# Performance work log

Measured on AMD Instinct MI355X. Metric: run time of the kernel, lower is better.

Reference implementation:

```python
import jax, jax.numpy as jnp
import numpy as np

B, F, L, P, H = 32, 64, 8192, 96, 8
HD = F // H
EPS_ATTN = 1e-6
EPS_REVIN = 1e-5
EPS_LN = 1e-5


def setup_inputs() -> dict:
    key = jax.random.key(0)
    ks = jax.random.split(key, 8)
    f32 = jnp.float32
    return {
        'x': jax.random.normal(ks[0], (B, F, L), dtype=f32),
        'gamma': jnp.ones((1, 1, F), dtype=f32),
        'beta': jnp.zeros((1, 1, F), dtype=f32),
        'ln_w': jnp.ones((F,), dtype=f32),
        'ln_b': jnp.zeros((F,), dtype=f32),
        'Wq': 0.05 * jax.random.normal(ks[1], (F, F), dtype=f32),
        'bq': jnp.zeros((F,), dtype=f32),
        'Wk': 0.05 * jax.random.normal(ks[2], (F, F), dtype=f32),
        'bk': jnp.zeros((F,), dtype=f32),
        'Wv': 0.05 * jax.random.normal(ks[3], (F, F), dtype=f32),
        'bv': jnp.zeros((F,), dtype=f32),
        'Wo': 0.05 * jax.random.normal(ks[4], (F, F), dtype=f32),
        'bo': jnp.zeros((F,), dtype=f32),
        'Wlin': 0.01 * jax.random.normal(ks[5], (P, L), dtype=f32),
        'blin': jnp.zeros((P,), dtype=f32),
        'Wp': 0.1 * jax.random.normal(ks[6], (1, F), dtype=f32),
        'bp': jnp.zeros((1,), dtype=f32),
    }


def _phi(t):
    # feature map: elu(x) + 1 (non-negative)
    return jax.nn.elu(t) + 1.0


def _layernorm(h, w, b):
    mu = jnp.mean(h, axis=-1, keepdims=True)
    var = jnp.mean(jnp.square(h - mu), axis=-1, keepdims=True)
    return (h - mu) * jax.lax.rsqrt(var + EPS_LN) * w + b


def reference(x, gamma, beta, ln_w, ln_b, Wq, bq, Wk, bk, Wv, bv, Wo, bo,
              Wlin, blin, Wp, bp):
    # (B, F, L) -> (B, L, F)
    xt = jnp.transpose(x, (0, 2, 1))
    # RevIN norm (stats over time axis, detached; torch std is unbiased ddof=1)
    mean = jax.lax.stop_gradient(jnp.mean(xt, axis=1, keepdims=True))
    std = jax.lax.stop_gradient(jnp.std(xt, axis=1, keepdims=True, ddof=1) + EPS_REVIN)
    xn = (xt - mean) / std * gamma + beta
    residual = xn
    h = _layernorm(xn, ln_w, ln_b)
    # Q/K/V projections (torch Linear: h @ W.T + b)
    Q = h @ Wq.T + bq
    K = h @ Wk.T + bk
    V = h @ Wv.T + bv
    # (B, L, F) -> (B, H, L, HD)
    def heads(t):
        return jnp.transpose(t.reshape(B, L, H, HD), (0, 2, 1, 3))
    Q, K, V = heads(Q), heads(K), heads(V)
    Q, K = _phi(Q), _phi(K)
    # linear attention: phi(Q) (phi(K)^T V) / (phi(Q) sum_n phi(K))
    KV = jnp.einsum('bhnd,bhne->bhde', K, V)           # (B,H,HD,HD)
    out = jnp.einsum('bhnd,bhde->bhne', Q, KV)          # (B,H,L,HD)
    Z = jnp.sum(K, axis=2)                              # (B,H,HD)
    normalizer = jnp.einsum('bhnd,bhd->bhn', Q, Z)[..., None] + EPS_ATTN
    out = out / normalizer
    out = jnp.transpose(out, (0, 2, 1, 3)).reshape(B, L, F)
    out = out @ Wo.T + bo
    y = out + residual                                  # (B, L, F)
    # temporal linear: (B, F, L) @ Wlin.T -> (B, F, P) -> (B, P, F)
    y = jnp.transpose(jnp.transpose(y, (0, 2, 1)) @ Wlin.T + blin, (0, 2, 1))
    # RevIN denorm
    y = (y - beta) / gamma
    y = y * std + mean
    # projector to scalar per step
    return (y @ Wp.T + bp)[..., 0]                      # (B, P)
```

## Files before the change

kernel.cpp:

```cpp
#include <hip/hip_runtime.h>
#include <cstddef>

#define NB 32
#define NF 64
#define NL 8192
#define NP 96
#define NH 8
#define TSPLIT 32

#define WS_MEAN 0
#define WS_STD  2048
#define WS_RSTD 4096
#define WS_KV   6144
#define WS_Z    22528
#define WS_OUT2 24576
#define WS_MUN  221184
#define WS_RSN  483328
#define WS_WLB  745472
#define WS_XNB  1138688
#define WS_YT   9527296

typedef __bf16 bfx8 __attribute__((ext_vector_type(8)));
typedef float f32x4 __attribute__((ext_vector_type(4)));
#define MFMA16(a, b, c) __builtin_amdgcn_mfma_f32_16x16x32_bf16((a), (b), (c), 0, 0, 0)

__device__ __forceinline__ unsigned short f2bf(float f) {
  unsigned u = __float_as_uint(f);
  unsigned r = u + 0x7FFFu + ((u >> 16) & 1u);
  return (unsigned short)(r >> 16);
}
__device__ __forceinline__ unsigned packbf2(float lo, float hi) {
  return (unsigned)f2bf(lo) | ((unsigned)f2bf(hi) << 16);
}
__device__ __forceinline__ float bflo(unsigned d) { return __uint_as_float(d << 16); }
__device__ __forceinline__ float bfhi(unsigned d) { return __uint_as_float(d & 0xFFFF0000u); }
__device__ __forceinline__ float bf1(unsigned short s) { return __uint_as_float(((unsigned)s) << 16); }

__device__ __forceinline__ bfx8 ldfrag(const unsigned short* p) {
  uint4 u = *(const uint4*)p;
  return __builtin_bit_cast(bfx8, u);
}

__global__ __launch_bounds__(256) void k_stats(const float* __restrict__ x,
                                               float* __restrict__ wmean,
                                               float* __restrict__ wstd,
                                               float* __restrict__ wrstd) {
  int bf = blockIdx.x;
  int tid = threadIdx.x;
  const float4* row4 = (const float4*)(x + (size_t)bf * NL);
  float s1 = 0.f, s2 = 0.f;
#pragma unroll
  for (int i = 0; i < NL / 4 / 256; i++) {
    float4 v = row4[tid + i * 256];
    s1 += v.x + v.y + v.z + v.w;
    s2 += v.x * v.x + v.y * v.y + v.z * v.z + v.w * v.w;
  }
  __shared__ float r1[256], r2[256];
  r1[tid] = s1; r2[tid] = s2;
  __syncthreads();
  for (int off = 128; off > 0; off >>= 1) {
    if (tid < off) { r1[tid] += r1[tid + off]; r2[tid] += r2[tid + off]; }
    __syncthreads();
  }
  if (tid == 0) {
    float m = r1[0] * (1.f / NL);
    float var = (r2[0] - (float)NL * m * m) * (1.f / (NL - 1));
    float sd = sqrtf(fmaxf(var, 0.f)) + 1e-5f;
    wmean[bf] = m;
    wstd[bf] = sd;
    wrstd[bf] = 1.f / sd;
  }
}

__global__ __launch_bounds__(256) void k_wlb(const float* __restrict__ Wlin,
                                             unsigned short* __restrict__ wlb) {
  int i = blockIdx.x * 256 + threadIdx.x;
  int p = i >> 10;
  int l8 = (i & 1023) * 8;
  float4 va = *(const float4*)&Wlin[(size_t)p * NL + l8];
  float4 vb = *(const float4*)&Wlin[(size_t)p * NL + l8 + 4];
  uint4 o;
  o.x = packbf2(va.x, va.y); o.y = packbf2(va.z, va.w);
  o.z = packbf2(vb.x, vb.y); o.w = packbf2(vb.z, vb.w);
  *(uint4*)&wlb[(((size_t)(l8 >> 5)) * NP + p) * 32 + (l8 & 31)] = o;
}

__global__ __launch_bounds__(256, 4) void k_kv(
    const float* __restrict__ x,
    const float* __restrict__ gamma, const float* __restrict__ beta,
    const float* __restrict__ lnw, const float* __restrict__ lnb,
    const float* __restrict__ Wk, const float* __restrict__ bk,
    const float* __restrict__ Wv, const float* __restrict__ bv,
    const float* __restrict__ wmean, const float* __restrict__ wrstd,
    float* __restrict__ wKV, float* __restrict__ wZ,
    float* __restrict__ wmun, float* __restrict__ wrsn,
    unsigned short* __restrict__ xnb) {
  __shared__ __align__(16) char smem[40960];
  unsigned short* hA  = (unsigned short*)smem;
  unsigned short* WkB = (unsigned short*)(smem + 18432);
  unsigned short* WvB = (unsigned short*)(smem + 27648);
  unsigned short* pK  = (unsigned short*)smem;
  unsigned short* pV  = (unsigned short*)(smem + 17408);
  float* SkT   = (float*)(smem + 36864);
  float* Tpart = (float*)(smem + 37888);
  float* mun   = (float*)(smem + 39936);
  float* rsn   = (float*)(smem + 40448);

  const int tid = threadIdx.x;
  const int b = blockIdx.x >> 6;
  const int tI = blockIdx.x & 63;
  const int L0 = tI * 128;
  const int lane = tid & 63, wv = tid >> 6;
  const int mm = lane & 15, qd = lane >> 4;

  {
    int jj = tid >> 2, g = tid & 3;
    int f0 = g * 16;
    float tkp = 0.f, tvp = 0.f;
#pragma unroll
    for (int i = 0; i < 4; i++) {
      int f = f0 + i * 4;
      float4 wk4 = *(const float4*)&Wk[jj * NF + f];
      float4 wv4 = *(const float4*)&Wv[jj * NF + f];
      float4 lw  = *(const float4*)&lnw[f];
      float4 lb  = *(const float4*)&lnb[f];
      uint2 pk2, pv2;
      pk2.x = packbf2(wk4.x * lw.x, wk4.y * lw.y);
      pk2.y = packbf2(wk4.z * lw.z, wk4.w * lw.w);
      pv2.x = packbf2(wv4.x * lw.x, wv4.y * lw.y);
      pv2.y = packbf2(wv4.z * lw.z, wv4.w * lw.w);
      *(uint2*)&WkB[jj * 72 + f] = pk2;
      *(uint2*)&WvB[jj * 72 + f] = pv2;
      tkp += lb.x * wk4.x + lb.y * wk4.y + lb.z * wk4.z + lb.w * wk4.w;
      tvp += lb.x * wv4.x + lb.y * wv4.y + lb.z * wv4.z + lb.w * wv4.w;
    }
    Tpart[g * 64 + jj] = tkp;
    Tpart[256 + g * 64 + jj] = tvp;
  }

  if (tid < 128) {
    float xn[NF];
    float mu = 0.f;
#pragma unroll
    for (int f = 0; f < NF; f++) {
      float v = x[((size_t)(b * NF + f)) * NL + L0 + tid];
      v = (v - wmean[b * NF + f]) * wrstd[b * NF + f] * gamma[f] + beta[f];
      xn[f] = v; mu += v;
    }
    mu *= (1.f / NF);
    float var = 0.f;
#pragma unroll
    for (int f = 0; f < NF; f++) { float d = xn[f] - mu; var += d * d; }
    float rs = rsqrtf(var * (1.f / NF) + 1e-5f);
    mun[tid] = mu; rsn[tid] = rs;
    wmun[(size_t)b * NL + L0 + tid] = mu;
    wrsn[(size_t)b * NL + L0 + tid] = rs;
    unsigned* hrow = (unsigned*)&hA[tid * 72];
#pragma unroll
    for (int f2 = 0; f2 < 32; f2++)
      hrow[f2] = packbf2(xn[2 * f2], xn[2 * f2 + 1]);
  }
  __syncthreads();

  {
    int row = tid >> 1, half = tid & 1;
    const uint4* s4 = (const uint4*)&hA[row * 72 + half * 32];
    uint4* d4 = (uint4*)(xnb + (((size_t)(b * 64 + tI) * 128 + row) * 64 + half * 32));
    d4[0] = s4[0]; d4[1] = s4[1]; d4[2] = s4[2]; d4[3] = s4[3];
  }

  if (tid < 128) {
    int sel = tid >> 6, j = tid & 63;
    const unsigned* wr = (const unsigned*)((sel ? WvB : WkB) + j * 72);
    float s = 0.f;
#pragma unroll
    for (int i = 0; i < 32; i++) { unsigned d = wr[i]; s += bflo(d) + bfhi(d); }
    float t = Tpart[sel * 256 + j] + Tpart[sel * 256 + 64 + j] +
              Tpart[sel * 256 + 128 + j] + Tpart[sel * 256 + 192 + j];
    t += sel ? bv[j] : bk[j];
    SkT[sel * 128 + j] = s;
    SkT[sel * 128 + 64 + j] = t;
  }
  __syncthreads();

  const f32x4 fz = {0.f, 0.f, 0.f, 0.f};
  f32x4 kacc[2][4], vacc[2][4];
#pragma unroll
  for (int i = 0; i < 2; i++)
#pragma unroll
    for (int jt = 0; jt < 4; jt++) { kacc[i][jt] = fz; vacc[i][jt] = fz; }

#pragma unroll
  for (int kc = 0; kc < 2; kc++) {
    bfx8 a0 = ldfrag(&hA[(wv * 32 + mm) * 72 + kc * 32 + qd * 8]);
    bfx8 a1 = ldfrag(&hA[(wv * 32 + 16 + mm) * 72 + kc * 32 + qd * 8]);
#pragma unroll
    for (int jt = 0; jt < 4; jt++) {
      bfx8 bkf = ldfrag(&WkB[(jt * 16 + mm) * 72 + kc * 32 + qd * 8]);
      bfx8 bvf = ldfrag(&WvB[(jt * 16 + mm) * 72 + kc * 32 + qd * 8]);
      kacc[0][jt] = MFMA16(a0, bkf, kacc[0][jt]);
      kacc[1][jt] = MFMA16(a1, bkf, kacc[1][jt]);
      vacc[0][jt] = MFMA16(a0, bvf, vacc[0][jt]);
      vacc[1][jt] = MFMA16(a1, bvf, vacc[1][jt]);
    }
  }

#pragma unroll
  for (int lt2 = 0; lt2 < 2; lt2++) {
    float4 mu4 = *(const float4*)&mun[wv * 32 + lt2 * 16 + qd * 4];
    float4 rs4 = *(const float4*)&rsn[wv * 32 + lt2 * 16 + qd * 4];
    float muv[4] = {mu4.x, mu4.y, mu4.z, mu4.w};
    float rsv[4] = {rs4.x, rs4.y, rs4.z, rs4.w};
#pragma unroll
    for (int jt = 0; jt < 4; jt++) {
      int j = jt * 16 + mm;
      float Sk = SkT[j], Tk = SkT[64 + j], Sv = SkT[128 + j], Tv = SkT[192 + j];
#pragma unroll
      for (int r = 0; r < 4; r++) {
        float kk = rsv[r] * (kacc[lt2][jt][r] - muv[r] * Sk) + Tk;
        kacc[lt2][jt][r] = (kk > 0.f) ? (kk + 1.f) : __expf(kk);
        vacc[lt2][jt][r] = rsv[r] * (vacc[lt2][jt][r] - muv[r] * Sv) + Tv;
      }
    }
  }
  __syncthreads();

#pragma unroll
  for (int lt2 = 0; lt2 < 2; lt2++) {
    int l0 = wv * 32 + lt2 * 16 + qd * 4;
#pragma unroll
    for (int jt = 0; jt < 4; jt++) {
      int j = jt * 16 + mm;
      uint2 dk, dv;
      dk.x = packbf2(kacc[lt2][jt][0], kacc[lt2][jt][1]);
      dk.y = packbf2(kacc[lt2][jt][2], kacc[lt2][jt][3]);
      dv.x = packbf2(vacc[lt2][jt][0], vacc[lt2][jt][1]);
      dv.y = packbf2(vacc[lt2][jt][2], vacc[lt2][jt][3]);
      *(uint2*)&pK[j * 136 + l0] = dk;
      *(uint2*)&pV[j * 136 + l0] = dv;
    }
  }
  __syncthreads();

  {
    f32x4 racc = fz;
#pragma unroll
    for (int kb = 0; kb < 4; kb++) {
      bfx8 ak = ldfrag(&pK[(wv * 16 + mm) * 136 + kb * 32 + qd * 8]);
      bfx8 bv8 = ldfrag(&pV[(wv * 16 + mm) * 136 + kb * 32 + qd * 8]);
      racc = MFMA16(ak, bv8, racc);
    }
    int eh = mm >> 3, e = mm & 7;
#pragma unroll
    for (int r = 0; r < 4; r++) {
      int row = qd * 4 + r;
      if ((row >> 3) == eh)
        atomicAdd(&wKV[(b * NH + wv * 2 + eh) * 64 + (row & 7) * 8 + e], racc[r]);
    }
  }
  if (tid < 64) {
    const unsigned* kr = (const unsigned*)&pK[tid * 136];
    float zs = 0.f;
#pragma unroll
    for (int i = 0; i < 64; i++) { unsigned d = kr[i]; zs += bflo(d) + bfhi(d); }
    atomicAdd(&wZ[b * 64 + tid], zs);
  }
}

__global__ __launch_bounds__(256, 3) void k_qy(
    const unsigned short* __restrict__ xnb,
    const float* __restrict__ lnw, const float* __restrict__ lnb,
    const float* __restrict__ Wq, const float* __restrict__ bq,
    const float* __restrict__ Wo, const float* __restrict__ bo,
    const float* __restrict__ wmun, const float* __restrict__ wrsn,
    const float* __restrict__ wKV, const float* __restrict__ wZ,
    unsigned short* __restrict__ ytb) {
  __shared__ __align__(16) char smem[41728];
  unsigned short* hA  = (unsigned short*)smem;
  unsigned short* qaA = (unsigned short*)smem;
  unsigned short* WqB = (unsigned short*)(smem + 18432);
  unsigned short* WoB = (unsigned short*)(smem + 27648);
  float* kvz   = (float*)(smem + 36864);
  float* mun   = (float*)(smem + 39168);
  float* rsn   = (float*)(smem + 39680);
  float* SqTq  = (float*)(smem + 40192);
  float* Tpart = (float*)(smem + 40704);

  const int tid = threadIdx.x;
  const int b = blockIdx.x >> 6;
  const int tI = blockIdx.x & 63;
  const int L0 = tI * 128;
  const int lane = tid & 63, wv = tid >> 6;
  const int mm = lane & 15, qd = lane >> 4;
  const unsigned short* xtile = xnb + (size_t)(b * 64 + tI) * 128 * 64;

  {
    int jj = tid >> 2, g = tid & 3;
    int f0 = g * 16;
    float tqp = 0.f;
#pragma unroll
    for (int i = 0; i < 4; i++) {
      int f = f0 + i * 4;
      float4 wq4 = *(const float4*)&Wq[jj * NF + f];
      float4 wo4 = *(const float4*)&Wo[jj * NF + f];
      float4 lw  = *(const float4*)&lnw[f];
      float4 lb  = *(const float4*)&lnb[f];
      uint2 pq2, po2;
      pq2.x = packbf2(wq4.x * lw.x, wq4.y * lw.y);
      pq2.y = packbf2(wq4.z * lw.z, wq4.w * lw.w);
      po2.x = packbf2(wo4.x, wo4.y);
      po2.y = packbf2(wo4.z, wo4.w);
      *(uint2*)&WqB[jj * 72 + f] = pq2;
      *(uint2*)&WoB[jj * 72 + f] = po2;
      tqp += lb.x * wq4.x + lb.y * wq4.y + lb.z * wq4.z + lb.w * wq4.w;
    }
    Tpart[g * 64 + jj] = tqp;
  }
  for (int i = tid; i < 576; i += 256)
    kvz[i] = (i < 512) ? wKV[b * 512 + i] : wZ[b * 64 + i - 512];
  {
    int row = tid >> 1, half = tid & 1;
    const uint4* s4 = (const uint4*)(xtile + (size_t)row * 64 + half * 32);
    uint4 u0 = s4[0], u1 = s4[1], u2 = s4[2], u3 = s4[3];
    uint4* d4 = (uint4*)&hA[row * 72 + half * 32];
    d4[0] = u0; d4[1] = u1; d4[2] = u2; d4[3] = u3;
  }
  if (tid < 128) {
    mun[tid] = wmun[(size_t)b * NL + L0 + tid];
    rsn[tid] = wrsn[(size_t)b * NL + L0 + tid];
  }
  __syncthreads();

  if (tid < 64) {
    const unsigned* wr = (const unsigned*)(WqB + tid * 72);
    float s = 0.f;
#pragma unroll
    for (int i = 0; i < 32; i++) { unsigned d = wr[i]; s += bflo(d) + bfhi(d); }
    float t = Tpart[tid] + Tpart[64 + tid] + Tpart[128 + tid] + Tpart[192 + tid] + bq[tid];
    SqTq[tid] = s; SqTq[64 + tid] = t;
  }
  __syncthreads();

  const f32x4 fz = {0.f, 0.f, 0.f, 0.f};

  {
    f32x4 qacc[2][4];
#pragma unroll
    for (int i = 0; i < 2; i++)
#pragma unroll
      for (int jt = 0; jt < 4; jt++) qacc[i][jt] = fz;
#pragma unroll
    for (int kc = 0; kc < 2; kc++) {
      bfx8 a0 = ldfrag(&hA[(wv * 32 + mm) * 72 + kc * 32 + qd * 8]);
      bfx8 a1 = ldfrag(&hA[(wv * 32 + 16 + mm) * 72 + kc * 32 + qd * 8]);
#pragma unroll
      for (int jt = 0; jt < 4; jt++) {
        bfx8 bqf = ldfrag(&WqB[(jt * 16 + mm) * 72 + kc * 32 + qd * 8]);
        qacc[0][jt] = MFMA16(a0, bqf, qacc[0][jt]);
        qacc[1][jt] = MFMA16(a1, bqf, qacc[1][jt]);
      }
    }
#pragma unroll
    for (int lt2 = 0; lt2 < 2; lt2++) {
      float4 mu4 = *(const float4*)&mun[wv * 32 + lt2 * 16 + qd * 4];
      float4 rs4 = *(const float4*)&rsn[wv * 32 + lt2 * 16 + qd * 4];
      float muv[4] = {mu4.x, mu4.y, mu4.z, mu4.w};
      float rsv[4] = {rs4.x, rs4.y, rs4.z, rs4.w};
      int l0 = wv * 32 + lt2 * 16 + qd * 4;
#pragma unroll
      for (int jt = 0; jt < 4; jt++) {
        int j = jt * 16 + mm;
        float Sj = SqTq[j], Tj = SqTq[64 + j];
#pragma unroll
        for (int r = 0; r < 4; r++) {
          float q = rsv[r] * (qacc[lt2][jt][r] - muv[r] * Sj) + Tj;
          q = (q > 0.f) ? (q + 1.f) : __expf(q);
          qaA[(l0 + r) * 72 + j] = f2bf(q);
        }
      }
    }
  }
  __syncthreads();

  {
    int lt = tid & 31, hd = tid >> 5;
    int lbase = lt * 4;
    float qv[4][8];
#pragma unroll
    for (int i = 0; i < 4; i++) {
      uint4 u = *(const uint4*)&qaA[(lbase + i) * 72 + hd * 8];
      qv[i][0] = bflo(u.x); qv[i][1] = bfhi(u.x);
      qv[i][2] = bflo(u.y); qv[i][3] = bfhi(u.y);
      qv[i][4] = bflo(u.z); qv[i][5] = bfhi(u.z);
      qv[i][6] = bflo(u.w); qv[i][7] = bfhi(u.w);
    }
    float att[4][8], nrm[4];
#pragma unroll
    for (int i = 0; i < 4; i++) {
      nrm[i] = 1e-6f;
#pragma unroll
      for (int e = 0; e < 8; e++) att[i][e] = 0.f;
    }
#pragma unroll
    for (int d = 0; d < 8; d++) {
      float zd = kvz[512 + hd * 8 + d];
      float4 kva = *(const float4*)&kvz[hd * 64 + d * 8];
      float4 kvb = *(const float4*)&kvz[hd * 64 + d * 8 + 4];
#pragma unroll
      for (int i = 0; i < 4; i++) {
        float qq = qv[i][d];
        nrm[i] = fmaf(qq, zd, nrm[i]);
        att[i][0] = fmaf(qq, kva.x, att[i][0]);
        att[i][1] = fmaf(qq, kva.y, att[i][1]);
        att[i][2] = fmaf(qq, kva.z, att[i][2]);
        att[i][3] = fmaf(qq, kva.w, att[i][3]);
        att[i][4] = fmaf(qq, kvb.x, att[i][4]);
        att[i][5] = fmaf(qq, kvb.y, att[i][5]);
        att[i][6] = fmaf(qq, kvb.z, att[i][6]);
        att[i][7] = fmaf(qq, kvb.w, att[i][7]);
      }
    }
#pragma unroll
    for (int i = 0; i < 4; i++) {
      float inv = 1.f / nrm[i];
      uint4 o;
      o.x = packbf2(att[i][0] * inv, att[i][1] * inv);
      o.y = packbf2(att[i][2] * inv, att[i][3] * inv);
      o.z = packbf2(att[i][4] * inv, att[i][5] * inv);
      o.w = packbf2(att[i][6] * inv, att[i][7] * inv);
      *(uint4*)&qaA[(lbase + i) * 72 + hd * 8] = o;
    }
  }
  __syncthreads();

  {
    f32x4 yacc[2][4];
#pragma unroll
    for (int i = 0; i < 2; i++)
#pragma unroll
      for (int ft = 0; ft < 4; ft++) yacc[i][ft] = fz;
#pragma unroll
    for (int ec = 0; ec < 2; ec++) {
      bfx8 a0 = ldfrag(&qaA[(wv * 32 + mm) * 72 + ec * 32 + qd * 8]);
      bfx8 a1 = ldfrag(&qaA[(wv * 32 + 16 + mm) * 72 + ec * 32 + qd * 8]);
#pragma unroll
      for (int ft = 0; ft < 4; ft++) {
        bfx8 bof = ldfrag(&WoB[(ft * 16 + mm) * 72 + ec * 32 + qd * 8]);
        yacc[0][ft] = MFMA16(a0, bof, yacc[0][ft]);
        yacc[1][ft] = MFMA16(a1, bof, yacc[1][ft]);
      }
    }
#pragma unroll
    for (int lt2 = 0; lt2 < 2; lt2++) {
      int l0 = wv * 32 + lt2 * 16 + qd * 4;
#pragma unroll
      for (int ft = 0; ft < 4; ft++) {
        int ff = ft * 16 + mm;
        float bof = bo[ff];
        float v0 = yacc[lt2][ft][0] + bf1(xtile[(size_t)(l0 + 0) * 64 + ff]) + bof;
        float v1 = yacc[lt2][ft][1] + bf1(xtile[(size_t)(l0 + 1) * 64 + ff]) + bof;
        float v2 = yacc[lt2][ft][2] + bf1(xtile[(size_t)(l0 + 2) * 64 + ff]) + bof;
        float v3 = yacc[lt2][ft][3] + bf1(xtile[(size_t)(l0 + 3) * 64 + ff]) + bof;
        uint2 o2;
        o2.x = packbf2(v0, v1);
        o2.y = packbf2(v2, v3);
        size_t idx = (((size_t)b * (NL / 32) + (L0 >> 5) + wv) * 64 + ff) * 32 + lt2 * 16 + qd * 4;
        *(uint2*)&ytb[idx] = o2;
      }
    }
  }
}

__global__ __launch_bounds__(256) void k_temporal(
    const unsigned short* __restrict__ ytb, const unsigned short* __restrict__ wlb,
    float* __restrict__ out2) {
  const int tid = threadIdx.x, lane = tid & 63, wvx = tid >> 6;
  const int mm = lane & 15, qd = lane >> 4;
  const int b = blockIdx.x / TSPLIT;
  const int kc = blockIdx.x % TSPLIT;
  const f32x4 fz = {0.f, 0.f, 0.f, 0.f};
  f32x4 acc[6];
#pragma unroll
  for (int pt = 0; pt < 6; pt++) acc[pt] = fz;

#pragma unroll 2
  for (int ks = 0; ks < 8; ks++) {
    int lg = kc * 8 + ks;
    bfx8 bfr = ldfrag(&ytb[(((size_t)b * (NL / 32) + lg) * 64 + wvx * 16 + mm) * 32 + qd * 8]);
#pragma unroll
    for (int pt = 0; pt < 6; pt++) {
      bfx8 afr = ldfrag(&wlb[((size_t)lg * NP + pt * 16 + mm) * 32 + qd * 8]);
      acc[pt] = MFMA16(afr, bfr, acc[pt]);
    }
  }
  const int ff = wvx * 16 + mm;
#pragma unroll
  for (int pt = 0; pt < 6; pt++) {
#pragma unroll
    for (int r = 0; r < 4; r++) {
      int p = pt * 16 + qd * 4 + r;
      atomicAdd(&out2[((size_t)(b * NP + p)) * NF + ff], acc[pt][r]);
    }
  }
}

__global__ __launch_bounds__(64) void k_final(
    const float* __restrict__ out2, const float* __restrict__ blin,
    const float* __restrict__ gamma, const float* __restrict__ beta,
    const float* __restrict__ wmean, const float* __restrict__ wstd,
    const float* __restrict__ Wp, const float* __restrict__ bp,
    float* __restrict__ out) {
  int b = blockIdx.x / NP;
  int p = blockIdx.x % NP;
  int f = threadIdx.x;
  float v = out2[((size_t)(b * NP + p)) * NF + f] + blin[p];
  v = (v - beta[f]) / gamma[f];
  v = v * wstd[b * NF + f] + wmean[b * NF + f];
  float s = v * Wp[f];
#pragma unroll
  for (int off = 32; off > 0; off >>= 1)
    s += __shfl_down(s, off, 64);
  if (f == 0) out[blockIdx.x] = s + bp[0];
}

extern "C" void kernel_launch(void* const* d_in, const int* in_sizes, int n_in,
                              void* d_out, int out_size, void* d_ws, size_t ws_size,
                              hipStream_t stream) {
  const float* x     = (const float*)d_in[0];
  const float* gamma = (const float*)d_in[1];
  const float* beta  = (const float*)d_in[2];
  const float* lnw   = (const float*)d_in[3];
  const float* lnb   = (const float*)d_in[4];
  const float* Wq    = (const float*)d_in[5];
  const float* bq    = (const float*)d_in[6];
  const float* Wk    = (const float*)d_in[7];
  const float* bk    = (const float*)d_in[8];
  const float* Wv    = (const float*)d_in[9];
  const float* bv    = (const float*)d_in[10];
  const float* Wo    = (const float*)d_in[11];
  const float* bo    = (const float*)d_in[12];
  const float* Wlin  = (const float*)d_in[13];
  const float* blin  = (const float*)d_in[14];
  const float* Wp    = (const float*)d_in[15];
  const float* bp    = (const float*)d_in[16];
  float* out = (float*)d_out;
  float* ws  = (float*)d_ws;

  float* wmean = ws + WS_MEAN;
  float* wstd  = ws + WS_STD;
  float* wrstd = ws + WS_RSTD;
  float* wKV   = ws + WS_KV;
  float* wZ    = ws + WS_Z;
  float* wout2 = ws + WS_OUT2;
  float* wmun  = ws + WS_MUN;
  float* wrsn  = ws + WS_RSN;
  unsigned short* wlb = (unsigned short*)(ws + WS_WLB);
  unsigned short* xnb = (unsigned short*)(ws + WS_XNB);
  unsigned short* ytb = (unsigned short*)(ws + WS_YT);

  (void)hipMemsetAsync(wKV, 0, (size_t)(16384 + 2048 + 196608) * sizeof(float), stream);

  k_stats<<<NB * NF, 256, 0, stream>>>(x, wmean, wstd, wrstd);
  k_wlb<<<NP * NL / 8 / 256, 256, 0, stream>>>(Wlin, wlb);
  k_kv<<<NB * 64, 256, 0, stream>>>(x, gamma, beta, lnw, lnb, Wk, bk, Wv, bv,
                                    wmean, wrstd, wKV, wZ, wmun, wrsn, xnb);
  k_qy<<<NB * 64, 256, 0, stream>>>(xnb, lnw, lnb, Wq, bq, Wo, bo,
                                    wmun, wrsn, wKV, wZ, ytb);
  k_temporal<<<NB * TSPLIT, 256, 0, stream>>>(ytb, wlb, wout2);
  k_final<<<NB * NP, 64, 0, stream>>>(wout2, blin, gamma, beta, wmean, wstd, Wp, bp, out);
}
```

Baseline: 237.1 us.

## Fuse stats, Wlin conversion and workspace zeroing into one prologue kernel; parallelize k_kv normalization

Merges the RevIN statistics kernel, the Wlin bf16 repack kernel and the workspace memset into a single k_pre launch, using wave shuffles instead of a shared-memory tree reduction. In k_kv the per-token normalization now uses all 256 threads, with two threads per token each handling half the features. It uses precomputed per-feature scale/shift pairs and a single-pass mean/variance. It also writes xnb directly from registers instead of copying back out of shared memory. The intent is to cut launch overhead and serialized work in the first kernels, at the cost of a less stable variance formula for the LayerNorm.

```diff
diff --git a/kernel.cpp b/kernel.cpp
--- a/kernel.cpp
+++ b/kernel.cpp
@@ -41,48 +41,51 @@
   return __builtin_bit_cast(bfx8, u);
 }
 
-__global__ __launch_bounds__(256) void k_stats(const float* __restrict__ x,
-                                               float* __restrict__ wmean,
-                                               float* __restrict__ wstd,
-                                               float* __restrict__ wrstd) {
-  int bf = blockIdx.x;
-  int tid = threadIdx.x;
-  const float4* row4 = (const float4*)(x + (size_t)bf * NL);
-  float s1 = 0.f, s2 = 0.f;
-#pragma unroll
-  for (int i = 0; i < NL / 4 / 256; i++) {
-    float4 v = row4[tid + i * 256];
-    s1 += v.x + v.y + v.z + v.w;
-    s2 += v.x * v.x + v.y * v.y + v.z * v.z + v.w * v.w;
-  }
-  __shared__ float r1[256], r2[256];
-  r1[tid] = s1; r2[tid] = s2;
-  __syncthreads();
-  for (int off = 128; off > 0; off >>= 1) {
-    if (tid < off) { r1[tid] += r1[tid + off]; r2[tid] += r2[tid + off]; }
+__global__ __launch_bounds__(256) void k_pre(
+    const float* __restrict__ x, const float* __restrict__ Wlin,
+    float* __restrict__ wmean, float* __restrict__ wstd, float* __restrict__ wrstd,
+    unsigned short* __restrict__ wlb, float* __restrict__ zz) {
+  __shared__ float r1[4], r2[4];
+  const int bid = blockIdx.x, tid = threadIdx.x;
+  if (bid < NB * NF) {
+    const float4* row4 = (const float4*)(x + (size_t)bid * NL);
+    float s1 = 0.f, s2 = 0.f;
+#pragma unroll
+    for (int i = 0; i < NL / 4 / 256; i++) {
+      float4 v = row4[tid + i * 256];
+      s1 += v.x + v.y + v.z + v.w;
+      s2 += v.x * v.x + v.y * v.y + v.z * v.z + v.w * v.w;
+    }
+#pragma unroll
+    for (int off = 32; off > 0; off >>= 1) {
+      s1 += __shfl_down(s1, off, 64);
+      s2 += __shfl_down(s2, off, 64);
+    }
+    if ((tid & 63) == 0) { r1[tid >> 6] = s1; r2[tid >> 6] = s2; }
     __syncthreads();
-  }
-  if (tid == 0) {
-    float m = r1[0] * (1.f / NL);
-    float var = (r2[0] - (float)NL * m * m) * (1.f / (NL - 1));
-    float sd = sqrtf(fmaxf(var, 0.f)) + 1e-5f;
-    wmean[bf] = m;
-    wstd[bf] = sd;
-    wrstd[bf] = 1.f / sd;
-  }
-}
-
-__global__ __launch_bounds__(256) void k_wlb(const float* __restrict__ Wlin,
-                                             unsigned short* __restrict__ wlb) {
-  int i = blockIdx.x * 256 + threadIdx.x;
-  int p = i >> 10;
-  int l8 = (i & 1023) * 8;
-  float4 va = *(const float4*)&Wlin[(size_t)p * NL + l8];
-  float4 vb = *(const float4*)&Wlin[(size_t)p * NL + l8 + 4];
-  uint4 o;
-  o.x = packbf2(va.x, va.y); o.y = packbf2(va.z, va.w);
-  o.z = packbf2(vb.x, vb.y); o.w = packbf2(vb.z, vb.w);
-  *(uint4*)&wlb[(((size_t)(l8 >> 5)) * NP + p) * 32 + (l8 & 31)] = o;
+    if (tid == 0) {
+      s1 = r1[0] + r1[1] + r1[2] + r1[3];
+      s2 = r2[0] + r2[1] + r2[2] + r2[3];
+      float m = s1 * (1.f / NL);
+      float var = (s2 - (float)NL * m * m) * (1.f / (NL - 1));
+      float sd = sqrtf(fmaxf(var, 0.f)) + 1e-5f;
+      wmean[bid] = m;
+      wstd[bid] = sd;
+      wrstd[bid] = 1.f / sd;
+    }
+    unsigned zi = (unsigned)bid * 256u + (unsigned)tid;
+    if (zi < 215040u) zz[zi] = 0.f;
+  } else {
+    int i = (bid - NB * NF) * 256 + tid;
+    int p = i >> 10;
+    int l8 = (i & 1023) * 8;
+    float4 va = *(const float4*)&Wlin[(size_t)p * NL + l8];
+    float4 vb = *(const float4*)&Wlin[(size_t)p * NL + l8 + 4];
+    uint4 o;
+    o.x = packbf2(va.x, va.y); o.y = packbf2(va.z, va.w);
+    o.z = packbf2(vb.x, vb.y); o.w = packbf2(vb.z, vb.w);
+    *(uint4*)&wlb[(((size_t)(l8 >> 5)) * NP + p) * 32 + (l8 & 31)] = o;
+  }
 }
 
 __global__ __launch_bounds__(256, 4) void k_kv(
@@ -95,16 +98,17 @@
     float* __restrict__ wKV, float* __restrict__ wZ,
     float* __restrict__ wmun, float* __restrict__ wrsn,
     unsigned short* __restrict__ xnb) {
-  __shared__ __align__(16) char smem[40960];
+  __shared__ __align__(16) char smem[39936];
   unsigned short* hA  = (unsigned short*)smem;
   unsigned short* WkB = (unsigned short*)(smem + 18432);
   unsigned short* WvB = (unsigned short*)(smem + 27648);
   unsigned short* pK  = (unsigned short*)smem;
   unsigned short* pV  = (unsigned short*)(smem + 17408);
-  float* SkT   = (float*)(smem + 36864);
-  float* Tpart = (float*)(smem + 37888);
-  float* mun   = (float*)(smem + 39936);
-  float* rsn   = (float*)(smem + 40448);
+  float* SkT  = (float*)(smem + 36864);
+  float* Tful = (float*)(smem + 37888);
+  float* mun  = (float*)(smem + 38400);
+  float* rsn  = (float*)(smem + 38912);
+  float* cbc  = (float*)(smem + 39424);
 
   const int tid = threadIdx.x;
   const int b = blockIdx.x >> 6;
@@ -113,6 +117,11 @@
   const int lane = tid & 63, wv = tid >> 6;
   const int mm = lane & 15, qd = lane >> 4;
 
+  if (tid < 64) {
+    float cb = wrstd[b * NF + tid] * gamma[tid];
+    cbc[2 * tid] = cb;
+    cbc[2 * tid + 1] = beta[tid] - wmean[b * NF + tid] * cb;
+  }
   {
     int jj = tid >> 2, g = tid & 3;
     int f0 = g * 16;
@@ -134,50 +143,57 @@
       tkp += lb.x * wk4.x + lb.y * wk4.y + lb.z * wk4.z + lb.w * wk4.w;
       tvp += lb.x * wv4.x + lb.y * wv4.y + lb.z * wv4.z + lb.w * wv4.w;
     }
-    Tpart[g * 64 + jj] = tkp;
-    Tpart[256 + g * 64 + jj] = tvp;
-  }
-
-  if (tid < 128) {
-    float xn[NF];
-    float mu = 0.f;
-#pragma unroll
-    for (int f = 0; f < NF; f++) {
-      float v = x[((size_t)(b * NF + f)) * NL + L0 + tid];
-      v = (v - wmean[b * NF + f]) * wrstd[b * NF + f] * gamma[f] + beta[f];
-      xn[f] = v; mu += v;
-    }
-    mu *= (1.f / NF);
-    float var = 0.f;
-#pragma unroll
-    for (int f = 0; f < NF; f++) { float d = xn[f] - mu; var += d * d; }
-    float rs = rsqrtf(var * (1.f / NF) + 1e-5f);
-    mun[tid] = mu; rsn[tid] = rs;
-    wmun[(size_t)b * NL + L0 + tid] = mu;
-    wrsn[(size_t)b * NL + L0 + tid] = rs;
-    unsigned* hrow = (unsigned*)&hA[tid * 72];
-#pragma unroll
-    for (int f2 = 0; f2 < 32; f2++)
-      hrow[f2] = packbf2(xn[2 * f2], xn[2 * f2 + 1]);
-  }
-  __syncthreads();
-
-  {
-    int row = tid >> 1, half = tid & 1;
-    const uint4* s4 = (const uint4*)&hA[row * 72 + half * 32];
-    uint4* d4 = (uint4*)(xnb + (((size_t)(b * 64 + tI) * 128 + row) * 64 + half * 32));
-    d4[0] = s4[0]; d4[1] = s4[1]; d4[2] = s4[2]; d4[3] = s4[3];
-  }
-
-  if (tid < 128) {
-    int sel = tid >> 6, j = tid & 63;
+    tkp += __shfl_xor(tkp, 1, 64); tkp += __shfl_xor(tkp, 2, 64);
+    tvp += __shfl_xor(tvp, 1, 64); tvp += __shfl_xor(tvp, 2, 64);
+    if (g == 0) { Tful[jj] = tkp; Tful[64 + jj] = tvp; }
+  }
+  __syncthreads();
+
+  {
+    const int l = tid >> 1, fh = tid & 1;
+    const float* xp = x + ((size_t)(b * NF + fh * 32)) * NL + L0 + l;
+    const float4* cb4 = (const float4*)&cbc[fh * 64];
+    float s1 = 0.f, s2 = 0.f;
+    unsigned pw[16];
+#pragma unroll
+    for (int f2 = 0; f2 < 16; f2++) {
+      float4 c = cb4[f2];
+      float v0 = xp[(size_t)(2 * f2) * NL];
+      float v1 = xp[(size_t)(2 * f2 + 1) * NL];
+      float a0 = fmaf(v0, c.x, c.y);
+      float a1 = fmaf(v1, c.z, c.w);
+      s1 += a0 + a1;
+      s2 += fmaf(a0, a0, a1 * a1);
+      pw[f2] = packbf2(a0, a1);
+    }
+    uint4 q[4];
+#pragma unroll
+    for (int i = 0; i < 4; i++) {
+      q[i].x = pw[4 * i]; q[i].y = pw[4 * i + 1];
+      q[i].z = pw[4 * i + 2]; q[i].w = pw[4 * i + 3];
+    }
+    uint4* hd = (uint4*)&hA[l * 72 + fh * 32];
+    uint4* gd = (uint4*)(xnb + (((size_t)(b * 64 + tI) * 128 + l) * 64 + fh * 32));
+#pragma unroll
+    for (int i = 0; i < 4; i++) { hd[i] = q[i]; gd[i] = q[i]; }
+    s1 += __shfl_xor(s1, 1, 64);
+    s2 += __shfl_xor(s2, 1, 64);
+    if (fh == 0) {
+      float mu = s1 * (1.f / NF);
+      float var = s2 * (1.f / NF) - mu * mu;
+      float rs = rsqrtf(fmaxf(var, 0.f) + 1e-5f);
+      mun[l] = mu; rsn[l] = rs;
+      wmun[(size_t)b * NL + L0 + l] = mu;
+      wrsn[(size_t)b * NL + L0 + l] = rs;
+    }
+  }
+  if (tid >= 128) {
+    int sel = (tid >> 6) - 2, j = tid & 63;
     const unsigned* wr = (const unsigned*)((sel ? WvB : WkB) + j * 72);
     float s = 0.f;
 #pragma unroll
     for (int i = 0; i < 32; i++) { unsigned d = wr[i]; s += bflo(d) + bfhi(d); }
-    float t = Tpart[sel * 256 + j] + Tpart[sel * 256 + 64 + j] +
-              Tpart[sel * 256 + 128 + j] + Tpart[sel * 256 + 192 + j];
-    t += sel ? bv[j] : bk[j];
+    float t = Tful[sel * 64 + j] + (sel ? bv[j] : bk[j]);
     SkT[sel * 128 + j] = s;
     SkT[sel * 128 + 64 + j] = t;
   }
@@ -558,10 +574,7 @@
   unsigned short* xnb = (unsigned short*)(ws + WS_XNB);
   unsigned short* ytb = (unsigned short*)(ws + WS_YT);
 
-  (void)hipMemsetAsync(wKV, 0, (size_t)(16384 + 2048 + 196608) * sizeof(float), stream);
-
-  k_stats<<<NB * NF, 256, 0, stream>>>(x, wmean, wstd, wrstd);
-  k_wlb<<<NP * NL / 8 / 256, 256, 0, stream>>>(Wlin, wlb);
+  k_pre<<<NB * NF + NP * NL / 8 / 256, 256, 0, stream>>>(x, Wlin, wmean, wstd, wrstd, wlb, wKV);
   k_kv<<<NB * 64, 256, 0, stream>>>(x, gamma, beta, lnw, lnb, Wk, bk, Wv, bv,
                                     wmean, wrstd, wKV, wZ, wmun, wrsn, xnb);
   k_qy<<<NB * 64, 256, 0, stream>>>(xnb, lnw, lnb, Wq, bq, Wo, bo,
```

Measured after the change: 227.6 us. -4.0%, faster.
